# Kernel tuning notes

Measured on AMD Instinct MI355X. Metric: run time of the kernel, lower is better.

Reference implementation:

```python
import jax, jax.numpy as jnp
import numpy as np

N, D_IN, D_OUT = 8192, 4096, 4096
ACT_BITS = 8


def setup_inputs() -> dict:
    key = jax.random.key(0)
    k1, k2, k3 = jax.random.split(key, 3)
    x = jax.random.normal(k1, (N, D_IN), dtype=jnp.float32)
    # ternary weight buffer in {-1, 0, +1} (stored as int8 in torch; int32 here)
    weight = jax.random.randint(k2, (D_OUT, D_IN), -1, 2, dtype=jnp.int32)
    weight_scale = jnp.array(0.05, dtype=jnp.float32)
    bias = jax.random.normal(k3, (D_OUT,), dtype=jnp.float32) * 0.01
    return {"x": x, "weight": weight, "weight_scale": weight_scale, "bias": bias}


def reference(x, weight, weight_scale, bias):
    qmax = 2.0 ** (ACT_BITS - 1) - 1.0   # 127
    qmin = -(2.0 ** (ACT_BITS - 1))      # -128
    # absmax activation quantization (eval-mode path of the module)
    scale = jnp.max(jnp.abs(x)) / qmax
    scale = jnp.where(scale == 0, jnp.float32(1.0), scale)
    x_int = jnp.clip(jnp.round(x / scale), qmin, qmax)
    # ternary matmul: pos_mask - neg_mask == weight itself for ternary values,
    # so F.linear(x, pos) - F.linear(x, neg) == x @ W^T
    w = weight.astype(jnp.float32)
    out = x_int @ w.T  # [N, D_OUT]
    out = out * weight_scale * scale
    return out + bias
```

## Files before the change

### kernel.cpp

```cpp
#include <hip/hip_runtime.h>
#include <hip/hip_bf16.h>

#define M_DIM 8192
#define N_DIM 4096
#define K_DIM 4096

typedef __attribute__((ext_vector_type(4))) int int4v;

__device__ __forceinline__ int quant4(float4 v, float rs) {
    float r0 = rintf(v.x * rs), r1 = rintf(v.y * rs);
    float r2 = rintf(v.z * rs), r3 = rintf(v.w * rs);
    int i0 = (int)fminf(127.0f, fmaxf(-128.0f, r0));
    int i1 = (int)fminf(127.0f, fmaxf(-128.0f, r1));
    int i2 = (int)fminf(127.0f, fmaxf(-128.0f, r2));
    int i3 = (int)fminf(127.0f, fmaxf(-128.0f, r3));
    return (i0 & 255) | ((i1 & 255) << 8) | ((i2 & 255) << 16) | (i3 << 24);
}

__device__ __forceinline__ int pack4i(int4 v) {
    return (v.x & 255) | ((v.y & 255) << 8) | ((v.z & 255) << 16) | (v.w << 24);
}

#define WCVT_BLOCKS 1024
#define ABS_BLOCKS 2048
__global__ void prep1_kernel(const float4* __restrict__ x,
                             const int4* __restrict__ w,
                             int* __restrict__ wq,
                             unsigned* __restrict__ amax) {
    if (blockIdx.x < WCVT_BLOCKS) {
        const int t = WCVT_BLOCKS * 256;
        const int n = (N_DIM * K_DIM) / 4;
        for (int i = blockIdx.x * 256 + threadIdx.x; i < n; i += 4 * t) {
            int4 a = w[i], b = w[i + t], c = w[i + 2 * t], d = w[i + 3 * t];
            wq[i] = pack4i(a);
            wq[i + t] = pack4i(b);
            wq[i + 2 * t] = pack4i(c);
            wq[i + 3 * t] = pack4i(d);
        }
    } else {
        const int t = ABS_BLOCKS * 256;
        const int n = (M_DIM * K_DIM) / 4;
        float m = 0.0f;
        for (int i = (blockIdx.x - WCVT_BLOCKS) * 256 + threadIdx.x; i < n;
             i += 4 * t) {
            float4 a = x[i], b = x[i + t], c = x[i + 2 * t], d = x[i + 3 * t];
            float ma = fmaxf(fmaxf(fabsf(a.x), fabsf(a.y)), fmaxf(fabsf(a.z), fabsf(a.w)));
            float mb = fmaxf(fmaxf(fabsf(b.x), fabsf(b.y)), fmaxf(fabsf(b.z), fabsf(b.w)));
            float mc = fmaxf(fmaxf(fabsf(c.x), fabsf(c.y)), fmaxf(fabsf(c.z), fabsf(c.w)));
            float md = fmaxf(fmaxf(fabsf(d.x), fabsf(d.y)), fmaxf(fabsf(d.z), fabsf(d.w)));
            m = fmaxf(m, fmaxf(fmaxf(ma, mb), fmaxf(mc, md)));
        }
        #pragma unroll
        for (int off = 32; off > 0; off >>= 1)
            m = fmaxf(m, __shfl_down(m, off, 64));
        __shared__ float sm[4];
        if ((threadIdx.x & 63) == 0) sm[threadIdx.x >> 6] = m;
        __syncthreads();
        if (threadIdx.x == 0) {
            float b = fmaxf(fmaxf(sm[0], sm[1]), fmaxf(sm[2], sm[3]));
            atomicMax(amax, __float_as_uint(b));
        }
    }
}

#define QUANT_BLOCKS 2048
__global__ void quant_kernel(const float4* __restrict__ x, int* __restrict__ q,
                             const unsigned* __restrict__ amax_u) {
    float amax = __uint_as_float(*amax_u);
    float scale = amax * (1.0f / 127.0f);
    if (scale == 0.0f) scale = 1.0f;
    const float rs = 1.0f / scale;
    const int t = QUANT_BLOCKS * 256;
    const int n = (M_DIM * K_DIM) / 4;
    for (int i = blockIdx.x * 256 + threadIdx.x; i < n; i += 4 * t) {
        float4 a = x[i], b = x[i + t], c = x[i + 2 * t], d = x[i + 3 * t];
        q[i] = quant4(a, rs);
        q[i + t] = quant4(b, rs);
        q[i + 2 * t] = quant4(c, rs);
        q[i + 3 * t] = quant4(d, rs);
    }
}

__device__ __forceinline__ void gload16(const char* g, char* l) {
    __builtin_amdgcn_global_load_lds(
        (const __attribute__((address_space(1))) unsigned int*)g,
        (__attribute__((address_space(3))) unsigned int*)l,
        16, 0, 0);
}

__global__ __launch_bounds__(256) void gemm_i8(
    const char* __restrict__ A,
    const char* __restrict__ B,
    float* __restrict__ C,
    const float* __restrict__ bias,
    const float* __restrict__ wscale,
    const unsigned* __restrict__ amax_u) {
    __shared__ __align__(16) char As[128 * 128];
    __shared__ __align__(16) char Bs[128 * 128];

    const int f = blockIdx.x;
    const int xcd = f & 7;
    const int slot = f >> 3;
    const int sm = slot >> 4;
    int sn = slot & 15;
    if (sm & 1) sn = 15 - sn;
    const int mBase = ((xcd >> 1) * 16 + sm) * 128;
    const int nBase = ((xcd & 1) * 16 + sn) * 128;

    const int t = threadIdx.x;
    const int w = t >> 6;
    const int l = t & 63;
    const int lm = l & 15;
    const int lq = l >> 4;
    const int wm = w >> 1;
    const int wn = w & 1;

    const char* aG[2];
    const char* bG[2];
    char* aL[2];
    char* bL[2];
    #pragma unroll
    for (int i = 0; i < 2; i++) {
        const int seg = 2 * w + i;
        aG[i] = A + (size_t)(mBase + seg * 16 + lm) * K_DIM + lq * 16;
        bG[i] = B + (size_t)(nBase + seg * 16 + lm) * K_DIM + lq * 16;
        aL[i] = As + seg * 2048;
        bL[i] = Bs + seg * 2048;
    }

    int4v acc[4][4];
    #pragma unroll
    for (int i = 0; i < 4; i++)
        #pragma unroll
        for (int j = 0; j < 4; j++)
            acc[i][j] = (int4v){0, 0, 0, 0};

    for (int kb = 0; kb < K_DIM; kb += 128) {
        #pragma unroll
        for (int i = 0; i < 2; i++) {
            #pragma unroll
            for (int s = 0; s < 2; s++) {
                gload16(aG[i] + kb + s * 64, aL[i] + s * 1024);
                gload16(bG[i] + kb + s * 64, bL[i] + s * 1024);
            }
        }
        __syncthreads();

        #pragma unroll
        for (int s = 0; s < 2; s++) {
            int4v af[4], bf[4];
            #pragma unroll
            for (int rt = 0; rt < 4; rt++) {
                af[rt] = *(const int4v*)(As + (wm * 4 + rt) * 2048 + s * 1024 + l * 16);
                bf[rt] = *(const int4v*)(Bs + (wn * 4 + rt) * 2048 + s * 1024 + l * 16);
            }
            #pragma unroll
            for (int rt = 0; rt < 4; rt++)
                #pragma unroll
                for (int ct = 0; ct < 4; ct++)
                    acc[rt][ct] = __builtin_amdgcn_mfma_i32_16x16x64_i8(
                        af[rt], bf[ct], acc[rt][ct], 0, 0, 0);
        }
        __syncthreads();
    }

    float amax = __uint_as_float(*amax_u);
    float scale = amax * (1.0f / 127.0f);
    if (scale == 0.0f) scale = 1.0f;
    const float s = wscale[0] * scale;

    #pragma unroll
    for (int ct = 0; ct < 4; ct++) {
        const int col = nBase + wn * 64 + ct * 16 + lm;
        const float bb = bias[col];
        #pragma unroll
        for (int rt = 0; rt < 4; rt++) {
            const int row0 = mBase + wm * 64 + rt * 16 + lq * 4;
            #pragma unroll
            for (int r = 0; r < 4; r++) {
                C[(size_t)(row0 + r) * N_DIM + col] = (float)acc[rt][ct][r] * s + bb;
            }
        }
    }
}

extern "C" void kernel_launch(void* const* d_in, const int* in_sizes, int n_in,
                              void* d_out, int out_size, void* d_ws, size_t ws_size,
                              hipStream_t stream) {
    const float* x      = (const float*)d_in[0];
    const int* weight   = (const int*)d_in[1];
    const float* wscale = (const float*)d_in[2];
    const float* bias   = (const float*)d_in[3];
    float* out          = (float*)d_out;

    unsigned char* ws = (unsigned char*)d_ws;
    unsigned* amax = (unsigned*)ws;
    char* Aq = (char*)(ws + 256);
    char* Wb = (char*)(ws + 256 + (size_t)M_DIM * K_DIM);

    hipMemsetAsync(amax, 0, sizeof(unsigned), stream);

    prep1_kernel<<<WCVT_BLOCKS + ABS_BLOCKS, 256, 0, stream>>>(
        (const float4*)x, (const int4*)weight, (int*)Wb, amax);
    quant_kernel<<<QUANT_BLOCKS, 256, 0, stream>>>((const float4*)x, (int*)Aq, amax);

    gemm_i8<<<2048, 256, 0, stream>>>(Aq, Wb, out, bias, wscale, amax);
}
```

Measured before the change: 542.6 us.

## Rewrite int8 GEMM with 256x256 tiles and four-stage LDS pipeline

The int8 MFMA GEMM moves from 128x128 tiles with 256 threads and one synchronous load per K step to 256x256 tiles with 512 threads. It uses a 4-deep ring of LDS buffers filled ahead by async global-to-LDS loads, split barriers, and s_setprio around the MFMA blocks. The aim is to overlap global loads with compute and to reuse each staged tile more, cutting global traffic and barrier stalls. In exchange it uses 128KB of LDS per block and more accumulator registers per thread, which limits occupancy.

```diff
diff --git a/kernel.cpp b/kernel.cpp
--- a/kernel.cpp
+++ b/kernel.cpp
@@ -88,81 +88,124 @@
         16, 0, 0);
 }
 
-__global__ __launch_bounds__(256) void gemm_i8(
+#define FENCE() asm volatile("" ::: "memory")
+#define BAR()                                \
+    do {                                     \
+        FENCE();                             \
+        __builtin_amdgcn_s_barrier();        \
+        FENCE();                             \
+    } while (0)
+
+__global__ __launch_bounds__(512, 2) void gemm_i8(
     const char* __restrict__ A,
     const char* __restrict__ B,
     float* __restrict__ C,
     const float* __restrict__ bias,
     const float* __restrict__ wscale,
     const unsigned* __restrict__ amax_u) {
-    __shared__ __align__(16) char As[128 * 128];
-    __shared__ __align__(16) char Bs[128 * 128];
+    __shared__ __align__(16) char L[4][32768];
 
     const int f = blockIdx.x;
     const int xcd = f & 7;
     const int slot = f >> 3;
-    const int sm = slot >> 4;
-    int sn = slot & 15;
-    if (sm & 1) sn = 15 - sn;
-    const int mBase = ((xcd >> 1) * 16 + sm) * 128;
-    const int nBase = ((xcd & 1) * 16 + sn) * 128;
+    const int sm = slot >> 3;
+    int sn = slot & 7;
+    if (sm & 1) sn = 7 - sn;
+    const int mBase = ((xcd >> 1) * 8 + sm) * 256;
+    const int nBase = ((xcd & 1) * 8 + sn) * 256;
 
     const int t = threadIdx.x;
     const int w = t >> 6;
     const int l = t & 63;
     const int lm = l & 15;
     const int lq = l >> 4;
-    const int wm = w >> 1;
-    const int wn = w & 1;
-
-    const char* aG[2];
-    const char* bG[2];
-    char* aL[2];
-    char* bL[2];
-    #pragma unroll
-    for (int i = 0; i < 2; i++) {
-        const int seg = 2 * w + i;
-        aG[i] = A + (size_t)(mBase + seg * 16 + lm) * K_DIM + lq * 16;
-        bG[i] = B + (size_t)(nBase + seg * 16 + lm) * K_DIM + lq * 16;
-        aL[i] = As + seg * 2048;
-        bL[i] = Bs + seg * 2048;
-    }
-
-    int4v acc[4][4];
-    #pragma unroll
-    for (int i = 0; i < 4; i++)
+    const int wm = w >> 2;
+    const int wn = w & 3;
+
+    const char* gp[4];
+    int lo[4];
+    #pragma unroll
+    for (int p = 0; p < 4; ++p) {
+        const int idx = p * 8 + w;
+        if (idx < 16) {
+            gp[p] = A + (size_t)(mBase + idx * 16 + lm) * K_DIM + lq * 16;
+            lo[p] = idx * 1024;
+        } else {
+            gp[p] = B + (size_t)(nBase + (idx - 16) * 16 + lm) * K_DIM + lq * 16;
+            lo[p] = 16384 + (idx - 16) * 1024;
+        }
+    }
+
+    #define STG(tt, p) gload16(gp[p] + (size_t)(tt) * 64, &L[(tt) & 3][0] + lo[p])
+
+    #pragma unroll
+    for (int tt = 0; tt < 3; ++tt) {
+        STG(tt, 0);
+        STG(tt, 1);
+        STG(tt, 2);
+        STG(tt, 3);
+    }
+
+    int4v acc[8][4];
+    #pragma unroll
+    for (int r = 0; r < 8; ++r)
         #pragma unroll
-        for (int j = 0; j < 4; j++)
-            acc[i][j] = (int4v){0, 0, 0, 0};
-
-    for (int kb = 0; kb < K_DIM; kb += 128) {
-        #pragma unroll
-        for (int i = 0; i < 2; i++) {
-            #pragma unroll
-            for (int s = 0; s < 2; s++) {
-                gload16(aG[i] + kb + s * 64, aL[i] + s * 1024);
-                gload16(bG[i] + kb + s * 64, bL[i] + s * 1024);
-            }
-        }
-        __syncthreads();
-
-        #pragma unroll
-        for (int s = 0; s < 2; s++) {
-            int4v af[4], bf[4];
-            #pragma unroll
-            for (int rt = 0; rt < 4; rt++) {
-                af[rt] = *(const int4v*)(As + (wm * 4 + rt) * 2048 + s * 1024 + l * 16);
-                bf[rt] = *(const int4v*)(Bs + (wn * 4 + rt) * 2048 + s * 1024 + l * 16);
-            }
-            #pragma unroll
-            for (int rt = 0; rt < 4; rt++)
-                #pragma unroll
-                for (int ct = 0; ct < 4; ct++)
-                    acc[rt][ct] = __builtin_amdgcn_mfma_i32_16x16x64_i8(
-                        af[rt], bf[ct], acc[rt][ct], 0, 0, 0);
-        }
-        __syncthreads();
-    }
+        for (int c = 0; c < 4; ++c)
+            acc[r][c] = (int4v){0, 0, 0, 0};
+
+    asm volatile("s_waitcnt vmcnt(8)" ::: "memory");
+    BAR();
+
+    #define KTILE(u, DO_STAGE, VMSTR)                                           \
+    do {                                                                        \
+        const char* lb = &L[(u) & 3][0];                                        \
+        const char* aB = lb + wm * 8192 + l * 16;                               \
+        const char* bB = lb + 16384 + wn * 4096 + l * 16;                       \
+        int4v af[4], bf[4];                                                     \
+                      \
+        _Pragma("unroll")                                                       \
+        for (int r = 0; r < 4; ++r) af[r] = *(const int4v*)(aB + r * 1024);     \
+        _Pragma("unroll")                                                       \
+        for (int c = 0; c < 4; ++c) bf[c] = *(const int4v*)(bB + c * 1024);     \
+        if (DO_STAGE) { STG((u) + 3, 0); STG((u) + 3, 1); }                     \
+        BAR();                                                                  \
+        __builtin_amdgcn_s_setprio(1);                                          \
+        _Pragma("unroll")                                                       \
+        for (int r = 0; r < 4; ++r)                                             \
+            _Pragma("unroll")                                                   \
+            for (int c = 0; c < 4; ++c)                                         \
+                acc[r][c] = __builtin_amdgcn_mfma_i32_16x16x64_i8(              \
+                    af[r], bf[c], acc[r][c], 0, 0, 0);                          \
+        __builtin_amdgcn_s_setprio(0);                                          \
+        BAR();                                                                  \
+                                              \
+        _Pragma("unroll")                                                       \
+        for (int r = 0; r < 4; ++r)                                             \
+            af[r] = *(const int4v*)(aB + (4 + r) * 1024);                       \
+        if (DO_STAGE) { STG((u) + 3, 2); STG((u) + 3, 3); }                     \
+        asm volatile("s_waitcnt " VMSTR ::: "memory");                          \
+        BAR();                                                                  \
+        __builtin_amdgcn_s_setprio(1);                                          \
+        _Pragma("unroll")                                                       \
+        for (int r = 0; r < 4; ++r)                                             \
+            _Pragma("unroll")                                                   \
+            for (int c = 0; c < 4; ++c)                                         \
+                acc[4 + r][c] = __builtin_amdgcn_mfma_i32_16x16x64_i8(          \
+                    af[r], bf[c], acc[4 + r][c], 0, 0, 0);                      \
+        __builtin_amdgcn_s_setprio(0);                                          \
+        BAR();                                                                  \
+    } while (0)
+
+    #pragma unroll 1
+    for (int u = 0; u < 61; ++u) {
+        KTILE(u, true, "vmcnt(8)");
+    }
+    KTILE(61, false, "vmcnt(4)");
+    KTILE(62, false, "vmcnt(0)");
+    KTILE(63, false, "vmcnt(0)");
+
+    #undef KTILE
+    #undef STG
 
     float amax = __uint_as_float(*amax_u);
     float scale = amax * (1.0f / 127.0f);
@@ -170,14 +213,14 @@
     const float s = wscale[0] * scale;
 
     #pragma unroll
-    for (int ct = 0; ct < 4; ct++) {
+    for (int ct = 0; ct < 4; ++ct) {
         const int col = nBase + wn * 64 + ct * 16 + lm;
         const float bb = bias[col];
         #pragma unroll
-        for (int rt = 0; rt < 4; rt++) {
-            const int row0 = mBase + wm * 64 + rt * 16 + lq * 4;
+        for (int rt = 0; rt < 8; ++rt) {
+            const int row0 = mBase + wm * 128 + rt * 16 + lq * 4;
             #pragma unroll
-            for (int r = 0; r < 4; r++) {
+            for (int r = 0; r < 4; ++r) {
                 C[(size_t)(row0 + r) * N_DIM + col] = (float)acc[rt][ct][r] * s + bb;
             }
         }
@@ -204,5 +247,5 @@
         (const float4*)x, (const int4*)weight, (int*)Wb, amax);
     quant_kernel<<<QUANT_BLOCKS, 256, 0, stream>>>((const float4*)x, (int*)Aq, amax);
 
-    gemm_i8<<<2048, 256, 0, stream>>>(Aq, Wb, out, bias, wscale, amax);
-}
+    gemm_i8<<<512, 512, 0, stream>>>(Aq, Wb, out, bias, wscale, amax);
+}
```

Result: faster. 437.7 us (-19.3%).

## Triple-buffer int8 GEMM with 256x128 tiles, 512 threads, and async prefetch

Applied to the files above, without the earlier changes.

The GEMM moves to 512-thread blocks computing 256x128 output tiles, with K steps of 64. Three LDS buffers let global-to-LDS loads run two steps ahead, gated by explicit vmcnt waits, and a single barrier per K step replaces the previous two. MFMA sections are wrapped in s_setprio. This is meant to hide global load latency and to reuse each B tile across more rows, at the cost of more LDS per block and fragile hand-counted wait and buffer-rotation logic.

```diff
diff --git a/kernel.cpp b/kernel.cpp
--- a/kernel.cpp
+++ b/kernel.cpp
@@ -88,15 +88,25 @@
         16, 0, 0);
 }
 
-__global__ __launch_bounds__(256) void gemm_i8(
+#define FENCE() asm volatile("" ::: "memory")
+#define BAR()                                \
+    do {                                     \
+        FENCE();                             \
+        __builtin_amdgcn_s_barrier();        \
+        FENCE();                             \
+    } while (0)
+
+#define BUF_SZ 24576
+#define LDS_SZ (3 * BUF_SZ)
+
+__global__ __launch_bounds__(512, 4) void gemm_i8(
     const char* __restrict__ A,
     const char* __restrict__ B,
     float* __restrict__ C,
     const float* __restrict__ bias,
     const float* __restrict__ wscale,
     const unsigned* __restrict__ amax_u) {
-    __shared__ __align__(16) char As[128 * 128];
-    __shared__ __align__(16) char Bs[128 * 128];
+    __shared__ __align__(16) char L[LDS_SZ];
 
     const int f = blockIdx.x;
     const int xcd = f & 7;
@@ -104,7 +114,7 @@
     const int sm = slot >> 4;
     int sn = slot & 15;
     if (sm & 1) sn = 15 - sn;
-    const int mBase = ((xcd >> 1) * 16 + sm) * 128;
+    const int mBase = ((xcd >> 1) * 8 + sm) * 256;
     const int nBase = ((xcd & 1) * 16 + sn) * 128;
 
     const int t = threadIdx.x;
@@ -115,18 +125,22 @@
     const int wm = w >> 1;
     const int wn = w & 1;
 
-    const char* aG[2];
-    const char* bG[2];
-    char* aL[2];
-    char* bL[2];
-    #pragma unroll
-    for (int i = 0; i < 2; i++) {
-        const int seg = 2 * w + i;
-        aG[i] = A + (size_t)(mBase + seg * 16 + lm) * K_DIM + lq * 16;
-        bG[i] = B + (size_t)(nBase + seg * 16 + lm) * K_DIM + lq * 16;
-        aL[i] = As + seg * 2048;
-        bL[i] = Bs + seg * 2048;
-    }
+    const char* gpA0 = A + (size_t)(mBase + w * 16 + lm) * K_DIM + lq * 16;
+    const char* gpA1 = gpA0 + (size_t)128 * K_DIM;
+    const char* gpB  = B + (size_t)(nBase + w * 16 + lm) * K_DIM + lq * 16;
+    const int loA0 = w * 1024;
+    const int loA1 = (8 + w) * 1024;
+    const int loB  = 16384 + w * 1024;
+
+    #define STG(tt, bufoff)                                      \
+    do {                                                         \
+        gload16(gpA0 + (size_t)(tt) * 64, L + (bufoff) + loA0);  \
+        gload16(gpA1 + (size_t)(tt) * 64, L + (bufoff) + loA1);  \
+        gload16(gpB  + (size_t)(tt) * 64, L + (bufoff) + loB);   \
+    } while (0)
+
+    STG(0, 0);
+    STG(1, BUF_SZ);
 
     int4v acc[4][4];
     #pragma unroll
@@ -135,34 +149,41 @@
         for (int j = 0; j < 4; j++)
             acc[i][j] = (int4v){0, 0, 0, 0};
 
-    for (int kb = 0; kb < K_DIM; kb += 128) {
-        #pragma unroll
-        for (int i = 0; i < 2; i++) {
-            #pragma unroll
-            for (int s = 0; s < 2; s++) {
-                gload16(aG[i] + kb + s * 64, aL[i] + s * 1024);
-                gload16(bG[i] + kb + s * 64, bL[i] + s * 1024);
-            }
-        }
-        __syncthreads();
-
-        #pragma unroll
-        for (int s = 0; s < 2; s++) {
-            int4v af[4], bf[4];
-            #pragma unroll
-            for (int rt = 0; rt < 4; rt++) {
-                af[rt] = *(const int4v*)(As + (wm * 4 + rt) * 2048 + s * 1024 + l * 16);
-                bf[rt] = *(const int4v*)(Bs + (wn * 4 + rt) * 2048 + s * 1024 + l * 16);
-            }
-            #pragma unroll
-            for (int rt = 0; rt < 4; rt++)
-                #pragma unroll
-                for (int ct = 0; ct < 4; ct++)
-                    acc[rt][ct] = __builtin_amdgcn_mfma_i32_16x16x64_i8(
-                        af[rt], bf[ct], acc[rt][ct], 0, 0, 0);
-        }
-        __syncthreads();
-    }
+    int cur = 0;
+    int curS = 2 * BUF_SZ;
+
+    #define KT(WSTR, DOSTG, u)                                              \
+    do {                                                                    \
+        asm volatile("s_waitcnt " WSTR ::: "memory");                       \
+        BAR();                                                              \
+        const char* aB = L + cur + wm * 4096 + l * 16;                      \
+        const char* bB = L + cur + 16384 + wn * 4096 + l * 16;              \
+        int4v af[4], bf[4];                                                 \
+        _Pragma("unroll")                                                   \
+        for (int r = 0; r < 4; ++r) af[r] = *(const int4v*)(aB + r * 1024); \
+        _Pragma("unroll")                                                   \
+        for (int c = 0; c < 4; ++c) bf[c] = *(const int4v*)(bB + c * 1024); \
+        if (DOSTG) STG((u) + 2, curS);                                      \
+        __builtin_amdgcn_s_setprio(1);                                      \
+        _Pragma("unroll")                                                   \
+        for (int r = 0; r < 4; ++r)                                         \
+            _Pragma("unroll")                                               \
+            for (int c = 0; c < 4; ++c)                                     \
+                acc[r][c] = __builtin_amdgcn_mfma_i32_16x16x64_i8(          \
+                    af[r], bf[c], acc[r][c], 0, 0, 0);                      \
+        __builtin_amdgcn_s_setprio(0);                                      \
+        cur += BUF_SZ;  if (cur == LDS_SZ) cur = 0;                         \
+        curS += BUF_SZ; if (curS == LDS_SZ) curS = 0;                       \
+    } while (0)
+
+    #pragma unroll 1
+    for (int u = 0; u < 63; ++u) {
+        KT("vmcnt(3)", u <= 61, u);
+    }
+    KT("vmcnt(0)", false, 63);
+
+    #undef KT
+    #undef STG
 
     float amax = __uint_as_float(*amax_u);
     float scale = amax * (1.0f / 127.0f);
@@ -170,14 +191,14 @@
     const float s = wscale[0] * scale;
 
     #pragma unroll
-    for (int ct = 0; ct < 4; ct++) {
+    for (int ct = 0; ct < 4; ++ct) {
         const int col = nBase + wn * 64 + ct * 16 + lm;
         const float bb = bias[col];
         #pragma unroll
-        for (int rt = 0; rt < 4; rt++) {
+        for (int rt = 0; rt < 4; ++rt) {
             const int row0 = mBase + wm * 64 + rt * 16 + lq * 4;
             #pragma unroll
-            for (int r = 0; r < 4; r++) {
+            for (int r = 0; r < 4; ++r) {
                 C[(size_t)(row0 + r) * N_DIM + col] = (float)acc[rt][ct][r] * s + bb;
             }
         }
@@ -204,5 +225,5 @@
         (const float4*)x, (const int4*)weight, (int*)Wb, amax);
     quant_kernel<<<QUANT_BLOCKS, 256, 0, stream>>>((const float4*)x, (int*)Aq, amax);
 
-    gemm_i8<<<2048, 256, 0, stream>>>(Aq, Wb, out, bias, wscale, amax);
-}
+    gemm_i8<<<1024, 512, 0, stream>>>(Aq, Wb, out, bias, wscale, amax);
+}
```

After: 487.5 us. 1.11x faster.
